# Performance work log

Hardware: AMD Instinct MI355X
Metric: run time of the kernel (lower is better)

The kernel has to match this reference:

```python
import jax, jax.numpy as jnp
import numpy as np

B = 4096
N_COL = 100      # all-numerical columns
N_COND = 64      # d*m = 4*16
D = 4
TOTAL = N_COL * N_COND   # 6400
N_RODT = TOTAL // D      # 1600
N_EST = 160              # max(2,int(sqrt(100))) * N_COND // D
N_FOREST = 100
N_HIDDEN = 128
N_CLASS = 10
EPS = 1e-5


def group_norm(x, w, b, groups):
    # x: [B, C] (spatial dim of 1 dropped); normalize within each channel group
    Bn, C = x.shape
    xg = x.reshape(Bn, groups, C // groups)
    mu = xg.mean(-1, keepdims=True)
    var = ((xg - mu) ** 2).mean(-1, keepdims=True)
    xn = ((xg - mu) * jax.lax.rsqrt(var + EPS)).reshape(Bn, C)
    return xn * w + b


def layer_norm(x, w, b):
    mu = x.mean(-1, keepdims=True)
    var = ((x - mu) ** 2).mean(-1, keepdims=True)
    return (x - mu) * jax.lax.rsqrt(var + EPS) * w + b


def setup_inputs() -> dict:
    key = jax.random.key(0)
    ks = jax.random.split(key, 16)
    s = 0.3  # weight scale
    x = jax.random.normal(ks[0], (B, N_COL), jnp.float32)
    w1 = jax.random.normal(ks[1], (N_COL, N_COND), jnp.float32) * s
    b1 = jax.random.normal(ks[2], (N_COL, N_COND), jnp.float32) * s
    perm = jax.random.permutation(ks[3], TOTAL)
    gn1_w = jnp.ones((TOTAL,), jnp.float32)
    gn1_b = jnp.zeros((TOTAL,), jnp.float32)
    conv2_w = jax.random.normal(ks[4], (N_RODT, D, D), jnp.float32) * s
    conv2_b = jax.random.normal(ks[5], (TOTAL,), jnp.float32) * s
    gn2_w = jnp.ones((TOTAL,), jnp.float32)
    gn2_b = jnp.zeros((TOTAL,), jnp.float32)
    conv3_w = jax.random.normal(ks[6], (N_RODT, D, 1), jnp.float32) * s
    conv3_b = jax.random.normal(ks[7], (N_RODT,), jnp.float32) * s
    # sample-without-replacement per forest (eval-mode fixed indices)
    swr = jax.vmap(lambda k: jax.random.permutation(k, N_RODT)[:N_EST])(
        jax.random.split(ks[8], N_FOREST))
    E = jax.random.normal(ks[9], (N_RODT, N_HIDDEN), jnp.float32)
    ln1_w = jnp.ones((N_HIDDEN,), jnp.float32)
    ln1_b = jnp.zeros((N_HIDDEN,), jnp.float32)
    fc1_w = jax.random.normal(ks[10], (N_HIDDEN, N_HIDDEN), jnp.float32) * (1.0 / np.sqrt(N_HIDDEN))
    fc1_b = jnp.zeros((N_HIDDEN,), jnp.float32)
    ln2_w = jnp.ones((N_HIDDEN,), jnp.float32)
    ln2_b = jnp.zeros((N_HIDDEN,), jnp.float32)
    fc2_w = jax.random.normal(ks[11], (N_HIDDEN, N_CLASS), jnp.float32) * (1.0 / np.sqrt(N_HIDDEN))
    fc2_b = jnp.zeros((N_CLASS,), jnp.float32)
    return dict(x=x, w1=w1, b1=b1, perm=perm, gn1_w=gn1_w, gn1_b=gn1_b,
                conv2_w=conv2_w, conv2_b=conv2_b, gn2_w=gn2_w, gn2_b=gn2_b,
                conv3_w=conv3_w, conv3_b=conv3_b, swr=swr, E=E,
                ln1_w=ln1_w, ln1_b=ln1_b, fc1_w=fc1_w, fc1_b=fc1_b,
                ln2_w=ln2_w, ln2_b=ln2_b, fc2_w=fc2_w, fc2_b=fc2_b)


def reference(x, w1, b1, perm, gn1_w, gn1_b, conv2_w, conv2_b, gn2_w, gn2_b,
              conv3_w, conv3_b, swr, E, ln1_w, ln1_b, fc1_w, fc1_b,
              ln2_w, ln2_b, fc2_w, fc2_b):
    b = x.shape[0]
    # --- ConditionGeneration (numerical path): per-column 1->n_cond group conv + sigmoid
    M = jax.nn.sigmoid(x[:, :, None] * w1[None] + b1[None])        # [B, n_col, n_cond]
    M = M.transpose(0, 2, 1)                                        # [B, n_cond, n_col]
    # --- rODTConstruction: flatten + fixed permutation
    O = M.reshape(b, -1)[:, perm]                                   # [B, total]
    # --- phi_2: GN -> grouped 4->4 conv -> ReLU -> GN -> grouped 4->1 conv
    h = group_norm(O, gn1_w, gn1_b, N_RODT)
    h = jnp.einsum('bgi,gio->bgo', h.reshape(b, N_RODT, D), conv2_w).reshape(b, TOTAL) + conv2_b
    h = jax.nn.relu(h)
    h = group_norm(h, gn2_w, gn2_b, N_RODT)
    w = jnp.einsum('bgi,gio->bgo', h.reshape(b, N_RODT, D), conv3_w)[..., 0] + conv3_b  # [B, n_rodt] (n_head=1)
    # --- rODT forest: gather estimators, softmax over estimators, weighted sum of rODT embeddings
    ws = jax.nn.softmax(w[:, swr], axis=2)                          # [B, n_forest, n_est]
    Ep = E[swr]                                                     # [n_forest, n_est, n_hidden]
    F = jnp.einsum('bfe,fed->bfd', ws, Ep)                          # [B, n_forest, n_hidden]
    # --- bagging MLP (dropout=0)
    h2 = layer_norm(F, ln1_w, ln1_b)
    h2 = jax.nn.relu(h2 @ fc1_w + fc1_b)
    h2 = layer_norm(h2, ln2_w, ln2_b)
    y_hat = h2 @ fc2_w + fc2_b                                      # [B, n_forest, n_class]
    return y_hat.mean(1)                                            # [B, n_class]
```

## Files before the change

kernel.cpp:

```cpp
#include <hip/hip_runtime.h>
#include <hip/hip_bf16.h>
#include <stdint.h>

#define NB 4096
#define NCOL 100
#define NCOND 64
#define NTOTAL 6400
#define NRODT 1600
#define NEST 160
#define NFOR 100
#define NHID 128
#define NCLS 10
#define GEPS 1e-5f

typedef __attribute__((ext_vector_type(8))) short short8;
typedef __attribute__((ext_vector_type(4))) float floatx4;

__device__ __forceinline__ unsigned f2bfu(float x) {
  union { float f; unsigned u; } v; v.f = x;
  return (v.u + 0x8000u) >> 16;
}
__device__ __forceinline__ float bf2f(unsigned short u) {
  union { unsigned u; float f; } v; v.u = ((unsigned)u) << 16;
  return v.f;
}

__device__ __forceinline__ float rowsum16(float v) {
  union { float f; int i; } a, t;
  a.f = v;
  t.i = __builtin_amdgcn_update_dpp(0, a.i, 0x128, 0xf, 0xf, true); a.f += t.f;
  t.i = __builtin_amdgcn_update_dpp(0, a.i, 0x124, 0xf, 0xf, true); a.f += t.f;
  t.i = __builtin_amdgcn_update_dpp(0, a.i, 0x122, 0xf, 0xf, true); a.f += t.f;
  t.i = __builtin_amdgcn_update_dpp(0, a.i, 0x121, 0xf, 0xf, true); a.f += t.f;
  return a.f;
}

__device__ __forceinline__ float bcast16(float v) {
  union { float f; int i; } a; a.f = v;
  a.i = __builtin_amdgcn_ds_swizzle(a.i, 0x0010);
  return a.f;
}

__global__ __launch_bounds__(256) void k01_prep(
    const float* __restrict__ x, const float* __restrict__ w1,
    const float* __restrict__ b1, const int* __restrict__ perm,
    const float* __restrict__ gn1w, const float* __restrict__ gn1b,
    const float* __restrict__ c2w, const float* __restrict__ c2b,
    const float* __restrict__ gn2w, const float* __restrict__ gn2b,
    const float* __restrict__ c3w, const float* __restrict__ c3b,
    const float* __restrict__ E, const int* __restrict__ swr,
    const float* __restrict__ fc1w, const float* __restrict__ fc2w,
    unsigned short* __restrict__ wT,
    unsigned short* __restrict__ Bf, unsigned short* __restrict__ W1f,
    unsigned short* __restrict__ W2f, float* __restrict__ out)
{
  __shared__ float xl[64 * NCOL];
  __shared__ int ridx[NEST];
  const int tid = threadIdx.x;
  const int blk = blockIdx.x;

  if (blk < 1600) {
    const int b0 = (blk & 63) * 64;
    const int g  = (blk >> 6) * 64 + (tid >> 2);
    const int i4 = tid & 3;
    for (int i = tid; i < 64 * NCOL; i += 256)
      xl[i] = x[(size_t)b0 * NCOL + i];
    __syncthreads();

    const int4 p4 = *(const int4*)(perm + 4 * g);
    const int pv[4] = {p4.x, p4.y, p4.z, p4.w};
    float w1v[4], b1v[4];
    int pc[4];
#pragma unroll
    for (int i = 0; i < 4; i++) {
      unsigned p = (unsigned)pv[i];
      unsigned j = p / 100u;
      unsigned cc = p - j * 100u;
      pc[i] = (int)cc;
      w1v[i] = w1[cc * NCOND + j];
      b1v[i] = b1[cc * NCOND + j];
    }
    const float4 g1w = *(const float4*)(gn1w + 4 * g);
    const float4 g1b = *(const float4*)(gn1b + 4 * g);
    const float4 cw0 = *(const float4*)(c2w + 16 * g);
    const float4 cw1 = *(const float4*)(c2w + 16 * g + 4);
    const float4 cw2 = *(const float4*)(c2w + 16 * g + 8);
    const float4 cw3 = *(const float4*)(c2w + 16 * g + 12);
    const float4 cbv = *(const float4*)(c2b + 4 * g);
    const float4 g2w = *(const float4*)(gn2w + 4 * g);
    const float4 g2b = *(const float4*)(gn2b + 4 * g);
    const float4 c3v = *(const float4*)(c3w + 4 * g);
    const float c3bv = c3b[g];

    for (int k = 0; k < 4; k++) {
      float v4[4];
#pragma unroll
      for (int j = 0; j < 4; j++) {
        const int bb = k * 16 + i4 * 4 + j;
        float O[4];
#pragma unroll
        for (int i = 0; i < 4; i++) {
          float a = xl[bb * NCOL + pc[i]] * w1v[i] + b1v[i];
          O[i] = 1.0f / (1.0f + __expf(-a));
        }
        float mu = 0.25f * (O[0] + O[1] + O[2] + O[3]);
        float d[4], var = 0.f;
#pragma unroll
        for (int i = 0; i < 4; i++) { d[i] = O[i] - mu; var += d[i] * d[i]; }
        float rs = rsqrtf(0.25f * var + GEPS);
        float xn0 = d[0] * rs * g1w.x + g1b.x;
        float xn1 = d[1] * rs * g1w.y + g1b.y;
        float xn2 = d[2] * rs * g1w.z + g1b.z;
        float xn3 = d[3] * rs * g1w.w + g1b.w;
        float h[4];
        h[0] = xn0*cw0.x + xn1*cw1.x + xn2*cw2.x + xn3*cw3.x + cbv.x;
        h[1] = xn0*cw0.y + xn1*cw1.y + xn2*cw2.y + xn3*cw3.y + cbv.y;
        h[2] = xn0*cw0.z + xn1*cw1.z + xn2*cw2.z + xn3*cw3.z + cbv.z;
        h[3] = xn0*cw0.w + xn1*cw1.w + xn2*cw2.w + xn3*cw3.w + cbv.w;
#pragma unroll
        for (int i = 0; i < 4; i++) h[i] = fmaxf(h[i], 0.f);
        float mu2 = 0.25f * (h[0] + h[1] + h[2] + h[3]);
        float e[4], var2 = 0.f;
#pragma unroll
        for (int i = 0; i < 4; i++) { e[i] = h[i] - mu2; var2 += e[i] * e[i]; }
        float rs2 = rsqrtf(0.25f * var2 + GEPS);
        float hn0 = e[0] * rs2 * g2w.x + g2b.x;
        float hn1 = e[1] * rs2 * g2w.y + g2b.y;
        float hn2 = e[2] * rs2 * g2w.z + g2b.z;
        float hn3 = e[3] * rs2 * g2w.w + g2b.w;
        v4[j] = hn0*c3v.x + hn1*c3v.y + hn2*c3v.z + hn3*c3v.w + c3bv;
      }
      uint2 pk;
      pk.x = f2bfu(__expf(v4[0])) | (f2bfu(__expf(v4[1])) << 16);
      pk.y = f2bfu(__expf(v4[2])) | (f2bfu(__expf(v4[3])) << 16);
      *(uint2*)(wT + (size_t)g * NB + b0 + k * 16 + i4 * 4) = pk;
    }
  } else if (blk < 1600 + NFOR) {
    const int fblk = blk - 1600;
    if (tid < NEST) ridx[tid] = swr[fblk * NEST + tid];
    __syncthreads();
    for (int m = tid; m < 2560; m += 256) {
      int lane = m & 63, rest = m >> 6;
      int kc = rest % 5, n = rest / 5;
      int q = lane >> 4, c = lane & 15;
      int e0 = kc * 32 + q * 8;
      int h = n * 16 + c;
      union { unsigned short v[8]; uint4 u; } t;
#pragma unroll
      for (int j = 0; j < 8; j++)
        t.v[j] = (unsigned short)f2bfu(E[(size_t)ridx[e0 + j] * NHID + h]);
      *(uint4*)(Bf + (size_t)fblk * 20480 + (size_t)m * 8) = t.u;
    }
  } else if (blk == 1600 + NFOR) {
    for (int m = tid; m < 2048; m += 256) {
      int lane = m & 63, rest = m >> 6;
      int kc = rest & 3, n = rest >> 2;
      int q = lane >> 4, c = lane & 15;
      int k0 = kc * 32 + q * 8;
      int o = n * 16 + c;
      union { unsigned short v[8]; uint4 u; } t;
#pragma unroll
      for (int j = 0; j < 8; j++)
        t.v[j] = (unsigned short)f2bfu(fc1w[(size_t)(k0 + j) * NHID + o]);
      *(uint4*)(W1f + (size_t)m * 8) = t.u;
    }
  } else if (blk == 1601 + NFOR) {
    for (int m = tid; m < 256; m += 256) {
      int lane = m & 63, kc = m >> 6;
      int q = lane >> 4, c = lane & 15;
      int k0 = kc * 32 + q * 8;
      union { unsigned short v[8]; uint4 u; } t;
#pragma unroll
      for (int j = 0; j < 8; j++)
        t.v[j] = (unsigned short)f2bfu(c < NCLS ? fc2w[(size_t)(k0 + j) * NCLS + c] : 0.f);
      *(uint4*)(W2f + (size_t)m * 8) = t.u;
    }
  } else {
    const int z = blk - (1602 + NFOR);
    float4 zz = make_float4(0.f, 0.f, 0.f, 0.f);
    for (int i = z * 256 + tid; i < NB * NCLS / 4; i += 3 * 256)
      ((float4*)out)[i] = zz;
  }
}

__global__ __launch_bounds__(256, 3) void k3_mfma(
    const unsigned short* __restrict__ wT,
    const int* __restrict__ swr,
    const unsigned short* __restrict__ Bf,
    const unsigned short* __restrict__ W1f,
    const unsigned short* __restrict__ W2f,
    const float* __restrict__ ln1w, const float* __restrict__ ln1b,
    const float* __restrict__ fc1b,
    const float* __restrict__ ln2w, const float* __restrict__ ln2b,
    const float* __restrict__ fc2b,
    float* __restrict__ out)
{
  __shared__ unsigned short lsA[128 * 168];

  const int tid = threadIdx.x;
  const int id  = blockIdx.y * 32 + blockIdx.x;
  const int xcd = id & 7;
  const int pos = id >> 3;
  const int f   = pos >> 2;
  const int b0  = (xcd * 4 + (pos & 3)) * 128;
  const int lane = tid & 63;
  const int wv = __builtin_amdgcn_readfirstlane(tid >> 6);
  const int c = lane & 15, q = lane >> 4;

  {
    const int* swf = swr + f * NEST + wv * 40;
    int idx[40];
#pragma unroll
    for (int e = 0; e < 40; e++) idx[e] = swf[e];

    const unsigned* wb32 = (const unsigned*)wT + (b0 >> 1) + lane;
    unsigned d[40];
#pragma unroll
    for (int e = 0; e < 40; e++)
      d[e] = wb32[(size_t)idx[e] * (NB / 2)];

    unsigned short* rp0 = lsA + (2 * lane) * 168 + wv * 40;
    unsigned short* rp1 = rp0 + 168;

#define PKLO(a, b) (((a) & 0xFFFFu) | ((b) << 16))
#define PKHI(a, b) (((a) >> 16) | ((b) & 0xFFFF0000u))
#pragma unroll
    for (int k = 0; k < 5; k++) {
      uint4 lo = {PKLO(d[8*k+0], d[8*k+1]), PKLO(d[8*k+2], d[8*k+3]),
                  PKLO(d[8*k+4], d[8*k+5]), PKLO(d[8*k+6], d[8*k+7])};
      uint4 hi = {PKHI(d[8*k+0], d[8*k+1]), PKHI(d[8*k+2], d[8*k+3]),
                  PKHI(d[8*k+4], d[8*k+5]), PKHI(d[8*k+6], d[8*k+7])};
      *(uint4*)(rp0 + k * 8) = lo;
      *(uint4*)(rp1 + k * 8) = hi;
    }
#undef PKLO
#undef PKHI
  }

  const unsigned short* bbase = Bf + (size_t)f * 20480 + lane * 8;
  short8 bp[8];
#pragma unroll
  for (int n = 0; n < 8; n++)
    bp[n] = *(const short8*)(bbase + n * 2560);

  __syncthreads();

  const unsigned short* pa0 = lsA + (wv * 16 + c) * 168 + q * 8;
  const unsigned short* pa1 = pa0 + 64 * 168;
  const short onev = (c == 0) ? (short)0x3F80 : (short)0;
  short8 bones;
#pragma unroll
  for (int j = 0; j < 8; j++) bones[j] = onev;

  floatx4 acc0[8], acc1[8];
  floatx4 accs0 = (floatx4){0.f, 0.f, 0.f, 0.f};
  floatx4 accs1 = (floatx4){0.f, 0.f, 0.f, 0.f};
  __builtin_amdgcn_s_setprio(1);
  {
    short8 a0 = *(const short8*)(pa0);
    short8 a1 = *(const short8*)(pa1);
#pragma unroll
    for (int n = 0; n < 8; n++) {
      acc0[n] = __builtin_amdgcn_mfma_f32_16x16x32_bf16(a0, bp[n], (floatx4){0.f,0.f,0.f,0.f}, 0, 0, 0);
      acc1[n] = __builtin_amdgcn_mfma_f32_16x16x32_bf16(a1, bp[n], (floatx4){0.f,0.f,0.f,0.f}, 0, 0, 0);
    }
    accs0 = __builtin_amdgcn_mfma_f32_16x16x32_bf16(a0, bones, accs0, 0, 0, 0);
    accs1 = __builtin_amdgcn_mfma_f32_16x16x32_bf16(a1, bones, accs1, 0, 0, 0);
  }
#pragma unroll
  for (int kc = 1; kc < 5; kc++) {
    short8 a0 = *(const short8*)(pa0 + kc * 32);
    short8 a1 = *(const short8*)(pa1 + kc * 32);
#pragma unroll
    for (int n = 0; n < 8; n++) {
      short8 b = *(const short8*)(bbase + n * 2560 + kc * 512);
      acc0[n] = __builtin_amdgcn_mfma_f32_16x16x32_bf16(a0, b, acc0[n], 0, 0, 0);
      acc1[n] = __builtin_amdgcn_mfma_f32_16x16x32_bf16(a1, b, acc1[n], 0, 0, 0);
    }
    accs0 = __builtin_amdgcn_mfma_f32_16x16x32_bf16(a0, bones, accs0, 0, 0, 0);
    accs1 = __builtin_amdgcn_mfma_f32_16x16x32_bf16(a1, bones, accs1, 0, 0, 0);
  }
  __builtin_amdgcn_s_setprio(0);

  {
    float lw[8], lb[8];
#pragma unroll
    for (int n = 0; n < 8; n++) { lw[n] = ln1w[n * 16 + c]; lb[n] = ln1b[n * 16 + c]; }
#pragma unroll
    for (int rr = 0; rr < 4; rr++) {
      {
        float st = bcast16(accs0[rr]);
        float s1 = 0.f, s2 = 0.f;
#pragma unroll
        for (int n = 0; n < 8; n++) { float v = acc0[n][rr]; s1 += v; s2 += v * v; }
        s1 = rowsum16(s1);
        s2 = rowsum16(s2);
        float mu = s1 * (1.f / 128.f);
        float var = fmaxf(s2 * (1.f / 128.f) - mu * mu, 0.f);
        float rs = rsqrtf(var + GEPS * st * st);
#pragma unroll
        for (int n = 0; n < 8; n++)
          acc0[n][rr] = (acc0[n][rr] - mu) * rs * lw[n] + lb[n];
      }
      {
        float st = bcast16(accs1[rr]);
        float s1 = 0.f, s2 = 0.f;
#pragma unroll
        for (int n = 0; n < 8; n++) { float v = acc1[n][rr]; s1 += v; s2 += v * v; }
        s1 = rowsum16(s1);
        s2 = rowsum16(s2);
        float mu = s1 * (1.f / 128.f);
        float var = fmaxf(s2 * (1.f / 128.f) - mu * mu, 0.f);
        float rs = rsqrtf(var + GEPS * st * st);
#pragma unroll
        for (int n = 0; n < 8; n++)
          acc1[n][rr] = (acc1[n][rr] - mu) * rs * lw[n] + lb[n];
      }
    }
  }

#pragma unroll
  for (int rr = 0; rr < 4; rr++)
#pragma unroll
    for (int n = 0; n < 8; n++) {
      lsA[(wv * 16 + q * 4 + rr) * 168 + n * 16 + c] =
          (unsigned short)f2bfu(acc0[n][rr]);
      lsA[(64 + wv * 16 + q * 4 + rr) * 168 + n * 16 + c] =
          (unsigned short)f2bfu(acc1[n][rr]);
    }

  {
    short8 a00 = *(const short8*)(pa0);
    short8 a01 = *(const short8*)(pa0 + 32);
    short8 a02 = *(const short8*)(pa0 + 64);
    short8 a03 = *(const short8*)(pa0 + 96);
    short8 a10 = *(const short8*)(pa1);
    short8 a11 = *(const short8*)(pa1 + 32);
    short8 a12 = *(const short8*)(pa1 + 64);
    short8 a13 = *(const short8*)(pa1 + 96);
    const unsigned short* w1p = W1f + lane * 8;
    __builtin_amdgcn_s_setprio(1);
#pragma unroll
    for (int n = 0; n < 8; n++) {
      const unsigned short* wp = w1p + n * 2048;
      short8 b0v = *(const short8*)(wp);
      short8 b1v = *(const short8*)(wp + 512);
      short8 b2v = *(const short8*)(wp + 1024);
      short8 b3v = *(const short8*)(wp + 1536);
      floatx4 t0 = __builtin_amdgcn_mfma_f32_16x16x32_bf16(a00, b0v, (floatx4){0.f,0.f,0.f,0.f}, 0, 0, 0);
      t0 = __builtin_amdgcn_mfma_f32_16x16x32_bf16(a01, b1v, t0, 0, 0, 0);
      t0 = __builtin_amdgcn_mfma_f32_16x16x32_bf16(a02, b2v, t0, 0, 0, 0);
      t0 = __builtin_amdgcn_mfma_f32_16x16x32_bf16(a03, b3v, t0, 0, 0, 0);
      floatx4 t1 = __builtin_amdgcn_mfma_f32_16x16x32_bf16(a10, b0v, (floatx4){0.f,0.f,0.f,0.f}, 0, 0, 0);
      t1 = __builtin_amdgcn_mfma_f32_16x16x32_bf16(a11, b1v, t1, 0, 0, 0);
      t1 = __builtin_amdgcn_mfma_f32_16x16x32_bf16(a12, b2v, t1, 0, 0, 0);
      t1 = __builtin_amdgcn_mfma_f32_16x16x32_bf16(a13, b3v, t1, 0, 0, 0);
      acc0[n] = t0;
      acc1[n] = t1;
    }
    __builtin_amdgcn_s_setprio(0);
  }

  {
    float fb[8], lw[8], lb[8];
#pragma unroll
    for (int n = 0; n < 8; n++) {
      fb[n] = fc1b[n * 16 + c];
      lw[n] = ln2w[n * 16 + c]; lb[n] = ln2b[n * 16 + c];
    }
#pragma unroll
    for (int rr = 0; rr < 4; rr++) {
      {
#pragma unroll
        for (int n = 0; n < 8; n++) acc0[n][rr] = fmaxf(acc0[n][rr] + fb[n], 0.f);
        float s1 = 0.f, s2 = 0.f;
#pragma unroll
        for (int n = 0; n < 8; n++) { float v = acc0[n][rr]; s1 += v; s2 += v * v; }
        s1 = rowsum16(s1);
        s2 = rowsum16(s2);
        float mu = s1 * (1.f / 128.f);
        float var = fmaxf(s2 * (1.f / 128.f) - mu * mu, 0.f);
        float rs = rsqrtf(var + GEPS);
#pragma unroll
        for (int n = 0; n < 8; n++)
          acc0[n][rr] = (acc0[n][rr] - mu) * rs * lw[n] + lb[n];
      }
      {
#pragma unroll
        for (int n = 0; n < 8; n++) acc1[n][rr] = fmaxf(acc1[n][rr] + fb[n], 0.f);
        float s1 = 0.f, s2 = 0.f;
#pragma unroll
        for (int n = 0; n < 8; n++) { float v = acc1[n][rr]; s1 += v; s2 += v * v; }
        s1 = rowsum16(s1);
        s2 = rowsum16(s2);
        float mu = s1 * (1.f / 128.f);
        float var = fmaxf(s2 * (1.f / 128.f) - mu * mu, 0.f);
        float rs = rsqrtf(var + GEPS);
#pragma unroll
        for (int n = 0; n < 8; n++)
          acc1[n][rr] = (acc1[n][rr] - mu) * rs * lw[n] + lb[n];
      }
    }
  }

#pragma unroll
  for (int rr = 0; rr < 4; rr++)
#pragma unroll
    for (int n = 0; n < 8; n++) {
      lsA[(wv * 16 + q * 4 + rr) * 168 + n * 16 + c] =
          (unsigned short)f2bfu(acc0[n][rr]);
      lsA[(64 + wv * 16 + q * 4 + rr) * 168 + n * 16 + c] =
          (unsigned short)f2bfu(acc1[n][rr]);
    }

  floatx4 o40 = (floatx4){0.f, 0.f, 0.f, 0.f};
  floatx4 o41 = (floatx4){0.f, 0.f, 0.f, 0.f};
#pragma unroll
  for (int kc = 0; kc < 4; kc++) {
    short8 a0 = *(const short8*)(pa0 + kc * 32);
    short8 a1 = *(const short8*)(pa1 + kc * 32);
    short8 b = *(const short8*)(W2f + kc * 512 + lane * 8);
    o40 = __builtin_amdgcn_mfma_f32_16x16x32_bf16(a0, b, o40, 0, 0, 0);
    o41 = __builtin_amdgcn_mfma_f32_16x16x32_bf16(a1, b, o41, 0, 0, 0);
  }
  if (c < NCLS) {
    float bias = fc2b[c];
#pragma unroll
    for (int rr = 0; rr < 4; rr++) {
      atomicAdd(out + (size_t)(b0 + wv * 16 + q * 4 + rr) * NCLS + c,
                (o40[rr] + bias) * 0.01f);
      atomicAdd(out + (size_t)(b0 + 64 + wv * 16 + q * 4 + rr) * NCLS + c,
                (o41[rr] + bias) * 0.01f);
    }
  }
}

extern "C" void kernel_launch(void* const* d_in, const int* in_sizes, int n_in,
                              void* d_out, int out_size, void* d_ws, size_t ws_size,
                              hipStream_t stream)
{
  (void)in_sizes; (void)n_in; (void)ws_size; (void)out_size;
  const float* x    = (const float*)d_in[0];
  const float* w1   = (const float*)d_in[1];
  const float* b1   = (const float*)d_in[2];
  const int*   perm = (const int*)d_in[3];
  const float* gn1w = (const float*)d_in[4];
  const float* gn1b = (const float*)d_in[5];
  const float* c2w  = (const float*)d_in[6];
  const float* c2b  = (const float*)d_in[7];
  const float* gn2w = (const float*)d_in[8];
  const float* gn2b = (const float*)d_in[9];
  const float* c3w  = (const float*)d_in[10];
  const float* c3b  = (const float*)d_in[11];
  const int*   swr  = (const int*)d_in[12];
  const float* E    = (const float*)d_in[13];
  const float* ln1w = (const float*)d_in[14];
  const float* ln1b = (const float*)d_in[15];
  const float* fc1w = (const float*)d_in[16];
  const float* fc1b = (const float*)d_in[17];
  const float* ln2w = (const float*)d_in[18];
  const float* ln2b = (const float*)d_in[19];
  const float* fc2w = (const float*)d_in[20];
  const float* fc2b = (const float*)d_in[21];
  float* out = (float*)d_out;

  const size_t W_BYTES = (size_t)NB * NRODT * 2;
  unsigned short* wTbuf = (unsigned short*)d_ws;
  unsigned short* Bfb   = (unsigned short*)((char*)d_ws + W_BYTES);
  unsigned short* W1fb  = (unsigned short*)((char*)d_ws + W_BYTES + 4096000);
  unsigned short* W2fb  = (unsigned short*)((char*)d_ws + W_BYTES + 4096000 + 32768);

  k01_prep<<<1600 + NFOR + 2 + 3, 256, 0, stream>>>(
      x, w1, b1, perm, gn1w, gn1b, c2w, c2b, gn2w, gn2b, c3w, c3b,
      E, swr, fc1w, fc2w, wTbuf, Bfb, W1fb, W2fb, out);
  dim3 g3(NB / 128, NFOR);
  k3_mfma<<<g3, 256, 0, stream>>>(wTbuf, swr, Bfb, W1fb, W2fb,
                                  ln1w, ln1b, fc1b, ln2w, ln2b, fc2b, out);
}
```

Baseline: 205.5 us.

## Process two forests per block, prefetching second forest's gathered scores during first

Each k3 block now handles two consecutive forests for the same batch tile, which halves the grid. The gather of the second forest's softmax logits from the transposed score buffer is issued into registers before the first forest's MFMA body runs. That gather latency can then overlap with compute, and block launch overhead is amortized. In exchange, per-thread register pressure rises (40 extra held values), which may lower occupancy or cause spills, and there are half as many blocks to spread across CUs.

```diff
diff --git a/kernel.cpp b/kernel.cpp
--- a/kernel.cpp
+++ b/kernel.cpp
@@ -183,9 +183,9 @@
   }
 }
 
-__global__ __launch_bounds__(256, 3) void k3_mfma(
-    const unsigned short* __restrict__ wT,
-    const int* __restrict__ swr,
+__device__ __forceinline__ void forest_body(
+    int f, int lane, int wv, int c, int q, int b0,
+    unsigned short* lsA,
     const unsigned short* __restrict__ Bf,
     const unsigned short* __restrict__ W1f,
     const unsigned short* __restrict__ W2f,
@@ -193,58 +193,9 @@
     const float* __restrict__ fc1b,
     const float* __restrict__ ln2w, const float* __restrict__ ln2b,
     const float* __restrict__ fc2b,
-    float* __restrict__ out)
+    float* __restrict__ out, const short8* bp)
 {
-  __shared__ unsigned short lsA[128 * 168];
-
-  const int tid = threadIdx.x;
-  const int id  = blockIdx.y * 32 + blockIdx.x;
-  const int xcd = id & 7;
-  const int pos = id >> 3;
-  const int f   = pos >> 2;
-  const int b0  = (xcd * 4 + (pos & 3)) * 128;
-  const int lane = tid & 63;
-  const int wv = __builtin_amdgcn_readfirstlane(tid >> 6);
-  const int c = lane & 15, q = lane >> 4;
-
-  {
-    const int* swf = swr + f * NEST + wv * 40;
-    int idx[40];
-#pragma unroll
-    for (int e = 0; e < 40; e++) idx[e] = swf[e];
-
-    const unsigned* wb32 = (const unsigned*)wT + (b0 >> 1) + lane;
-    unsigned d[40];
-#pragma unroll
-    for (int e = 0; e < 40; e++)
-      d[e] = wb32[(size_t)idx[e] * (NB / 2)];
-
-    unsigned short* rp0 = lsA + (2 * lane) * 168 + wv * 40;
-    unsigned short* rp1 = rp0 + 168;
-
-#define PKLO(a, b) (((a) & 0xFFFFu) | ((b) << 16))
-#define PKHI(a, b) (((a) >> 16) | ((b) & 0xFFFF0000u))
-#pragma unroll
-    for (int k = 0; k < 5; k++) {
-      uint4 lo = {PKLO(d[8*k+0], d[8*k+1]), PKLO(d[8*k+2], d[8*k+3]),
-                  PKLO(d[8*k+4], d[8*k+5]), PKLO(d[8*k+6], d[8*k+7])};
-      uint4 hi = {PKHI(d[8*k+0], d[8*k+1]), PKHI(d[8*k+2], d[8*k+3]),
-                  PKHI(d[8*k+4], d[8*k+5]), PKHI(d[8*k+6], d[8*k+7])};
-      *(uint4*)(rp0 + k * 8) = lo;
-      *(uint4*)(rp1 + k * 8) = hi;
-    }
-#undef PKLO
-#undef PKHI
-  }
-
   const unsigned short* bbase = Bf + (size_t)f * 20480 + lane * 8;
-  short8 bp[8];
-#pragma unroll
-  for (int n = 0; n < 8; n++)
-    bp[n] = *(const short8*)(bbase + n * 2560);
-
-  __syncthreads();
-
   const unsigned short* pa0 = lsA + (wv * 16 + c) * 168 + q * 8;
   const unsigned short* pa1 = pa0 + 64 * 168;
   const short onev = (c == 0) ? (short)0x3F80 : (short)0;
@@ -433,6 +384,108 @@
                 (o41[rr] + bias) * 0.01f);
     }
   }
+}
+
+__global__ __launch_bounds__(256, 3) void k3_mfma(
+    const unsigned short* __restrict__ wT,
+    const int* __restrict__ swr,
+    const unsigned short* __restrict__ Bf,
+    const unsigned short* __restrict__ W1f,
+    const unsigned short* __restrict__ W2f,
+    const float* __restrict__ ln1w, const float* __restrict__ ln1b,
+    const float* __restrict__ fc1b,
+    const float* __restrict__ ln2w, const float* __restrict__ ln2b,
+    const float* __restrict__ fc2b,
+    float* __restrict__ out)
+{
+  __shared__ unsigned short lsA[128 * 168];
+
+  const int tid = threadIdx.x;
+  const int id  = blockIdx.y * 32 + blockIdx.x;
+  const int xcd = id & 7;
+  const int pos = id >> 3;
+  const int f0  = (pos >> 2) * 2;
+  const int b0  = (xcd * 4 + (pos & 3)) * 128;
+  const int lane = tid & 63;
+  const int wv = __builtin_amdgcn_readfirstlane(tid >> 6);
+  const int c = lane & 15, q = lane >> 4;
+
+  const unsigned* wb32 = (const unsigned*)wT + (b0 >> 1) + lane;
+  unsigned short* rp0 = lsA + (2 * lane) * 168 + wv * 40;
+  unsigned short* rp1 = rp0 + 168;
+
+#define PKLO(a, b) (((a) & 0xFFFFu) | ((b) << 16))
+#define PKHI(a, b) (((a) >> 16) | ((b) & 0xFFFF0000u))
+
+  {
+    const int* swf = swr + f0 * NEST + wv * 40;
+    int idx[40];
+#pragma unroll
+    for (int e = 0; e < 40; e++) idx[e] = swf[e];
+    unsigned d[40];
+#pragma unroll
+    for (int e = 0; e < 40; e++)
+      d[e] = wb32[(size_t)idx[e] * (NB / 2)];
+#pragma unroll
+    for (int k = 0; k < 5; k++) {
+      uint4 lo = {PKLO(d[8*k+0], d[8*k+1]), PKLO(d[8*k+2], d[8*k+3]),
+                  PKLO(d[8*k+4], d[8*k+5]), PKLO(d[8*k+6], d[8*k+7])};
+      uint4 hi = {PKHI(d[8*k+0], d[8*k+1]), PKHI(d[8*k+2], d[8*k+3]),
+                  PKHI(d[8*k+4], d[8*k+5]), PKHI(d[8*k+6], d[8*k+7])};
+      *(uint4*)(rp0 + k * 8) = lo;
+      *(uint4*)(rp1 + k * 8) = hi;
+    }
+  }
+
+  unsigned d1[40];
+  {
+    const int* swf1 = swr + (f0 + 1) * NEST + wv * 40;
+    int idx1[40];
+#pragma unroll
+    for (int e = 0; e < 40; e++) idx1[e] = swf1[e];
+#pragma unroll
+    for (int e = 0; e < 40; e++)
+      d1[e] = wb32[(size_t)idx1[e] * (NB / 2)];
+  }
+  __builtin_amdgcn_sched_barrier(0);
+
+  short8 bp0[8];
+  {
+    const unsigned short* bb = Bf + (size_t)f0 * 20480 + lane * 8;
+#pragma unroll
+    for (int n = 0; n < 8; n++) bp0[n] = *(const short8*)(bb + n * 2560);
+  }
+
+  __syncthreads();
+
+  forest_body(f0, lane, wv, c, q, b0, lsA, Bf, W1f, W2f,
+              ln1w, ln1b, fc1b, ln2w, ln2b, fc2b, out, bp0);
+
+  short8 bp1[8];
+  {
+    const unsigned short* bb = Bf + (size_t)(f0 + 1) * 20480 + lane * 8;
+#pragma unroll
+    for (int n = 0; n < 8; n++) bp1[n] = *(const short8*)(bb + n * 2560);
+  }
+
+  __syncthreads();
+
+#pragma unroll
+  for (int k = 0; k < 5; k++) {
+    uint4 lo = {PKLO(d1[8*k+0], d1[8*k+1]), PKLO(d1[8*k+2], d1[8*k+3]),
+                PKLO(d1[8*k+4], d1[8*k+5]), PKLO(d1[8*k+6], d1[8*k+7])};
+    uint4 hi = {PKHI(d1[8*k+0], d1[8*k+1]), PKHI(d1[8*k+2], d1[8*k+3]),
+                PKHI(d1[8*k+4], d1[8*k+5]), PKHI(d1[8*k+6], d1[8*k+7])};
+    *(uint4*)(rp0 + k * 8) = lo;
+    *(uint4*)(rp1 + k * 8) = hi;
+  }
+#undef PKLO
+#undef PKHI
+
+  __syncthreads();
+
+  forest_body(f0 + 1, lane, wv, c, q, b0, lsA, Bf, W1f, W2f,
+              ln1w, ln1b, fc1b, ln2w, ln2b, fc2b, out, bp1);
 }
 
 extern "C" void kernel_launch(void* const* d_in, const int* in_sizes, int n_in,
@@ -473,7 +526,7 @@
   k01_prep<<<1600 + NFOR + 2 + 3, 256, 0, stream>>>(
       x, w1, b1, perm, gn1w, gn1b, c2w, c2b, gn2w, gn2b, c3w, c3b,
       E, swr, fc1w, fc2w, wTbuf, Bfb, W1fb, W2fb, out);
-  dim3 g3(NB / 128, NFOR);
+  dim3 g3(NB / 128, NFOR / 2);
   k3_mfma<<<g3, 256, 0, stream>>>(wTbuf, swr, Bfb, W1fb, W2fb,
                                   ln1w, ln1b, fc1b, ln2w, ln2b, fc2b, out);
 }
```

Measured after the change: 280.0 us. 1.36x slower.

## Gather MFMA A-fragments directly into registers, skip LDS staging

Applied to the files above, without the earlier changes.

The gathered softmax-weight tile is now loaded straight from global memory into the MFMA A-operand registers in fragment layout, using per-lane 16-bit loads. This removes the LDS write/read round trip and the block barrier before the first GEMM. LDS shrinks to a 136-element row stride since only the later stages use it, which may raise occupancy. The cost is many more narrow, less coalesced global loads and extra registers to hold all five K-chunks. The barrier between writing and reading LDS in later stages now relies on each wave touching only its own rows.

```diff
diff --git a/kernel.cpp b/kernel.cpp
--- a/kernel.cpp
+++ b/kernel.cpp
@@ -195,7 +195,7 @@
     const float* __restrict__ fc2b,
     float* __restrict__ out)
 {
-  __shared__ unsigned short lsA[128 * 168];
+  __shared__ unsigned short lsA[128 * 136];
 
   const int tid = threadIdx.x;
   const int id  = blockIdx.y * 32 + blockIdx.x;
@@ -207,46 +207,36 @@
   const int wv = __builtin_amdgcn_readfirstlane(tid >> 6);
   const int c = lane & 15, q = lane >> 4;
 
+  short8 a0f[5], a1f[5];
   {
-    const int* swf = swr + f * NEST + wv * 40;
-    int idx[40];
-#pragma unroll
-    for (int e = 0; e < 40; e++) idx[e] = swf[e];
-
-    const unsigned* wb32 = (const unsigned*)wT + (b0 >> 1) + lane;
-    unsigned d[40];
-#pragma unroll
-    for (int e = 0; e < 40; e++)
-      d[e] = wb32[(size_t)idx[e] * (NB / 2)];
-
-    unsigned short* rp0 = lsA + (2 * lane) * 168 + wv * 40;
-    unsigned short* rp1 = rp0 + 168;
-
-#define PKLO(a, b) (((a) & 0xFFFFu) | ((b) << 16))
-#define PKHI(a, b) (((a) >> 16) | ((b) & 0xFFFF0000u))
-#pragma unroll
-    for (int k = 0; k < 5; k++) {
-      uint4 lo = {PKLO(d[8*k+0], d[8*k+1]), PKLO(d[8*k+2], d[8*k+3]),
-                  PKLO(d[8*k+4], d[8*k+5]), PKLO(d[8*k+6], d[8*k+7])};
-      uint4 hi = {PKHI(d[8*k+0], d[8*k+1]), PKHI(d[8*k+2], d[8*k+3]),
-                  PKHI(d[8*k+4], d[8*k+5]), PKHI(d[8*k+6], d[8*k+7])};
-      *(uint4*)(rp0 + k * 8) = lo;
-      *(uint4*)(rp1 + k * 8) = hi;
-    }
-#undef PKLO
-#undef PKHI
+    const int* swq = swr + f * NEST + q * 8;
+    int4 iva[5], ivb[5];
+#pragma unroll
+    for (int kc = 0; kc < 5; kc++) {
+      iva[kc] = *(const int4*)(swq + kc * 32);
+      ivb[kc] = *(const int4*)(swq + kc * 32 + 4);
+    }
+    const unsigned short* wcol = wT + b0 + wv * 16 + c;
+#pragma unroll
+    for (int kc = 0; kc < 5; kc++) {
+      int e[8] = {iva[kc].x, iva[kc].y, iva[kc].z, iva[kc].w,
+                  ivb[kc].x, ivb[kc].y, ivb[kc].z, ivb[kc].w};
+      unsigned short t0[8], t1[8];
+#pragma unroll
+      for (int j = 0; j < 8; j++) {
+        const unsigned short* p = wcol + (size_t)e[j] * NB;
+        t0[j] = p[0];
+        t1[j] = p[64];
+      }
+#pragma unroll
+      for (int j = 0; j < 8; j++) {
+        a0f[kc][j] = (short)t0[j];
+        a1f[kc][j] = (short)t1[j];
+      }
+    }
   }
 
   const unsigned short* bbase = Bf + (size_t)f * 20480 + lane * 8;
-  short8 bp[8];
-#pragma unroll
-  for (int n = 0; n < 8; n++)
-    bp[n] = *(const short8*)(bbase + n * 2560);
-
-  __syncthreads();
-
-  const unsigned short* pa0 = lsA + (wv * 16 + c) * 168 + q * 8;
-  const unsigned short* pa1 = pa0 + 64 * 168;
   const short onev = (c == 0) ? (short)0x3F80 : (short)0;
   short8 bones;
 #pragma unroll
@@ -256,29 +246,24 @@
   floatx4 accs0 = (floatx4){0.f, 0.f, 0.f, 0.f};
   floatx4 accs1 = (floatx4){0.f, 0.f, 0.f, 0.f};
   __builtin_amdgcn_s_setprio(1);
-  {
-    short8 a0 = *(const short8*)(pa0);
-    short8 a1 = *(const short8*)(pa1);
-#pragma unroll
-    for (int n = 0; n < 8; n++) {
-      acc0[n] = __builtin_amdgcn_mfma_f32_16x16x32_bf16(a0, bp[n], (floatx4){0.f,0.f,0.f,0.f}, 0, 0, 0);
-      acc1[n] = __builtin_amdgcn_mfma_f32_16x16x32_bf16(a1, bp[n], (floatx4){0.f,0.f,0.f,0.f}, 0, 0, 0);
-    }
-    accs0 = __builtin_amdgcn_mfma_f32_16x16x32_bf16(a0, bones, accs0, 0, 0, 0);
-    accs1 = __builtin_amdgcn_mfma_f32_16x16x32_bf16(a1, bones, accs1, 0, 0, 0);
-  }
+#pragma unroll
+  for (int n = 0; n < 8; n++) {
+    short8 b = *(const short8*)(bbase + n * 2560);
+    acc0[n] = __builtin_amdgcn_mfma_f32_16x16x32_bf16(a0f[0], b, (floatx4){0.f,0.f,0.f,0.f}, 0, 0, 0);
+    acc1[n] = __builtin_amdgcn_mfma_f32_16x16x32_bf16(a1f[0], b, (floatx4){0.f,0.f,0.f,0.f}, 0, 0, 0);
+  }
+  accs0 = __builtin_amdgcn_mfma_f32_16x16x32_bf16(a0f[0], bones, accs0, 0, 0, 0);
+  accs1 = __builtin_amdgcn_mfma_f32_16x16x32_bf16(a1f[0], bones, accs1, 0, 0, 0);
 #pragma unroll
   for (int kc = 1; kc < 5; kc++) {
-    short8 a0 = *(const short8*)(pa0 + kc * 32);
-    short8 a1 = *(const short8*)(pa1 + kc * 32);
 #pragma unroll
     for (int n = 0; n < 8; n++) {
       short8 b = *(const short8*)(bbase + n * 2560 + kc * 512);
-      acc0[n] = __builtin_amdgcn_mfma_f32_16x16x32_bf16(a0, b, acc0[n], 0, 0, 0);
-      acc1[n] = __builtin_amdgcn_mfma_f32_16x16x32_bf16(a1, b, acc1[n], 0, 0, 0);
-    }
-    accs0 = __builtin_amdgcn_mfma_f32_16x16x32_bf16(a0, bones, accs0, 0, 0, 0);
-    accs1 = __builtin_amdgcn_mfma_f32_16x16x32_bf16(a1, bones, accs1, 0, 0, 0);
+      acc0[n] = __builtin_amdgcn_mfma_f32_16x16x32_bf16(a0f[kc], b, acc0[n], 0, 0, 0);
+      acc1[n] = __builtin_amdgcn_mfma_f32_16x16x32_bf16(a1f[kc], b, acc1[n], 0, 0, 0);
+    }
+    accs0 = __builtin_amdgcn_mfma_f32_16x16x32_bf16(a0f[kc], bones, accs0, 0, 0, 0);
+    accs1 = __builtin_amdgcn_mfma_f32_16x16x32_bf16(a1f[kc], bones, accs1, 0, 0, 0);
   }
   __builtin_amdgcn_s_setprio(0);
 
@@ -323,11 +308,14 @@
   for (int rr = 0; rr < 4; rr++)
 #pragma unroll
     for (int n = 0; n < 8; n++) {
-      lsA[(wv * 16 + q * 4 + rr) * 168 + n * 16 + c] =
+      lsA[(wv * 16 + q * 4 + rr) * 136 + n * 16 + c] =
           (unsigned short)f2bfu(acc0[n][rr]);
-      lsA[(64 + wv * 16 + q * 4 + rr) * 168 + n * 16 + c] =
+      lsA[(64 + wv * 16 + q * 4 + rr) * 136 + n * 16 + c] =
           (unsigned short)f2bfu(acc1[n][rr]);
     }
+
+  const unsigned short* pa0 = lsA + (wv * 16 + c) * 136 + q * 8;
+  const unsigned short* pa1 = pa0 + 64 * 136;
 
   {
     short8 a00 = *(const short8*)(pa0);
@@ -407,9 +395,9 @@
   for (int rr = 0; rr < 4; rr++)
 #pragma unroll
     for (int n = 0; n < 8; n++) {
-      lsA[(wv * 16 + q * 4 + rr) * 168 + n * 16 + c] =
+      lsA[(wv * 16 + q * 4 + rr) * 136 + n * 16 + c] =
           (unsigned short)f2bfu(acc0[n][rr]);
-      lsA[(64 + wv * 16 + q * 4 + rr) * 168 + n * 16 + c] =
+      lsA[(64 + wv * 16 + q * 4 + rr) * 136 + n * 16 + c] =
           (unsigned short)f2bfu(acc1[n][rr]);
     }
 
```

Measured after the change: 223.8 us. 1.09x slower.
